# Kernel optimization log

Measured on AMD Instinct MI355X. Metric: run time of the kernel, lower is better.

## Reference

```python
import jax, jax.numpy as jnp
import numpy as np

KSIZE = (15, 15)
SIGMA = (3.0, 3.0)


def _gaussian_kernel1d(kernel_size, sigma):
    ksize_half = (kernel_size - 1) * 0.5
    x = jnp.linspace(-ksize_half, ksize_half, kernel_size, dtype=jnp.float32)
    pdf = jnp.exp(-0.5 * (x / sigma) ** 2)
    return pdf / pdf.sum()


def setup_inputs() -> dict:
    key = jax.random.key(0)
    img = jax.random.normal(key, (8192, 8192), dtype=jnp.float32)
    # kernel = outer(kernel1d_y, kernel1d_x), matching torch.mm(y[:,None], x[None,:])
    k1d_x = _gaussian_kernel1d(KSIZE[0], SIGMA[0])
    k1d_y = _gaussian_kernel1d(KSIZE[1], SIGMA[1])
    kernel = jnp.outer(k1d_y, k1d_x)  # [kh, kw]
    return {"input": img, "kernel": kernel, "stride": 1}


def reference(input, kernel, stride):
    # forward(): squeeze -> custom mirror pad (== reflect, excludes edge) -> valid strided conv
    kh, kw = kernel.shape
    ph, pw = kh // 2, kw // 2
    x = jnp.pad(input, ((ph, ph), (pw, pw)), mode="reflect")  # matches the flip-based pad()
    # single-channel 2D cross-correlation, VALID padding, given stride
    out = jax.lax.conv_general_dilated(
        x[None, None, :, :],            # [1,1,H+2ph,W+2pw]
        kernel[None, None, :, :],       # [1,1,kh,kw]
        window_strides=(stride, stride),
        padding="VALID",
    )
    return out[0, 0]
```

## Files before the change

kernel.cpp:

```cpp
#include <hip/hip_runtime.h>

#define IMG_W 8192
#define IMG_H 8192
#define KS 15
#define RAD 7
#define TW 64
#define TH 64
#define BLOCK 256
#define SIN_W (TW + 2*RAD)
#define SIN_H (TH + 2*RAD)
#define SIN_STRIDE 80
#define MID_STRIDE TW

__device__ __forceinline__ int reflect_idx(int p, int n) {
    if (p < 0) p = -p;
    if (p >= n) p = 2 * n - 2 - p;
    return p;
}

__global__ __launch_bounds__(BLOCK)
void gauss15_fused(const float* __restrict__ in,
                   const float* __restrict__ k2d,
                   float* __restrict__ out) {
    __shared__ float s_in[SIN_H * SIN_STRIDE];
    __shared__ float s_mid[SIN_H * MID_STRIDE];
    __shared__ float s_kx[KS];
    __shared__ float s_ky[KS];

    const int t = threadIdx.x;
    const int col0 = blockIdx.x * TW;
    const int row0 = blockIdx.y * TH;

    if (t < KS) {
        float sx = 0.f, sy = 0.f;
        #pragma unroll
        for (int i = 0; i < KS; i++) {
            sx += k2d[i * KS + t];
            sy += k2d[t * KS + i];
        }
        s_kx[t] = sx;
        s_ky[t] = sy;
    }

    for (int idx = t; idx < SIN_H * SIN_W; idx += BLOCK) {
        int r = idx / SIN_W;
        int c = idx - r * SIN_W;
        int gr = reflect_idx(row0 - RAD + r, IMG_H);
        int gc = reflect_idx(col0 - RAD + c, IMG_W);
        s_in[r * SIN_STRIDE + c] = in[gr * IMG_W + gc];
    }
    __syncthreads();

    float kx[KS], ky[KS];
    #pragma unroll
    for (int i = 0; i < KS; i++) { kx[i] = s_kx[i]; ky[i] = s_ky[i]; }

    for (int idx = t; idx < SIN_H * (TW / 4); idx += BLOCK) {
        int r = idx >> 4;
        int cg = idx & 15;
        const float* rowp = &s_in[r * SIN_STRIDE + cg * 4];
        float f[20];
        *(float4*)(f + 0)  = *(const float4*)(rowp + 0);
        *(float4*)(f + 4)  = *(const float4*)(rowp + 4);
        *(float4*)(f + 8)  = *(const float4*)(rowp + 8);
        *(float4*)(f + 12) = *(const float4*)(rowp + 12);
        *(float4*)(f + 16) = *(const float4*)(rowp + 16);
        float a0 = 0.f, a1 = 0.f, a2 = 0.f, a3 = 0.f;
        #pragma unroll
        for (int j = 0; j < KS; j++) {
            float w = kx[j];
            a0 += f[j + 0] * w;
            a1 += f[j + 1] * w;
            a2 += f[j + 2] * w;
            a3 += f[j + 3] * w;
        }
        *(float4*)&s_mid[r * MID_STRIDE + cg * 4] = make_float4(a0, a1, a2, a3);
    }
    __syncthreads();

    const int cg = t & 15;
    const int rg = t >> 4;
    const int c = cg * 4;
    const int r0 = rg * 4;

    float4 acc[4];
    #pragma unroll
    for (int q = 0; q < 4; q++) acc[q] = make_float4(0.f, 0.f, 0.f, 0.f);

    #pragma unroll
    for (int i = 0; i < KS + 3; i++) {
        float4 v = *(const float4*)&s_mid[(r0 + i) * MID_STRIDE + c];
        #pragma unroll
        for (int q = 0; q < 4; q++) {
            int j = i - q;
            if (j >= 0 && j < KS) {
                float w = ky[j];
                acc[q].x += v.x * w;
                acc[q].y += v.y * w;
                acc[q].z += v.z * w;
                acc[q].w += v.w * w;
            }
        }
    }

    #pragma unroll
    for (int q = 0; q < 4; q++) {
        *(float4*)&out[(size_t)(row0 + r0 + q) * IMG_W + col0 + c] = acc[q];
    }
}

extern "C" void kernel_launch(void* const* d_in, const int* in_sizes, int n_in,
                              void* d_out, int out_size, void* d_ws, size_t ws_size,
                              hipStream_t stream) {
    const float* img = (const float*)d_in[0];
    const float* k2d = (const float*)d_in[1];
    float* out = (float*)d_out;

    dim3 grid(IMG_W / TW, IMG_H / TH);
    gauss15_fused<<<grid, BLOCK, 0, stream>>>(img, k2d, out);
}
```

Baseline: 518.7 us.

## Replace shared-memory tiled separable conv with register-streaming row kernel

Each thread now owns 4 output columns across a 1024-wide by 64-tall block. It streams input rows straight from global memory and does the horizontal pass in registers. The vertical pass uses a 15-entry rotating float4 accumulator ring kept in registers. This drops the shared-memory staging, both __syncthreads, and the intermediate buffer, and reduces the halo overhead, which was about 1.5x reads on 64x64 tiles. The costs are heavy register pressure and a grid of only 1024 blocks, and it relies on L1/L2 to serve the overlapping column reads between neighbouring threads.

```diff
diff --git a/kernel.cpp b/kernel.cpp
--- a/kernel.cpp
+++ b/kernel.cpp
@@ -4,13 +4,9 @@
 #define IMG_H 8192
 #define KS 15
 #define RAD 7
-#define TW 64
-#define TH 64
+#define TW_BLK 1024
+#define TH_BLK 64
 #define BLOCK 256
-#define SIN_W (TW + 2*RAD)
-#define SIN_H (TH + 2*RAD)
-#define SIN_STRIDE 80
-#define MID_STRIDE TW
 
 __device__ __forceinline__ int reflect_idx(int p, int n) {
     if (p < 0) p = -p;
@@ -18,95 +14,128 @@
     return p;
 }
 
-__global__ __launch_bounds__(BLOCK)
-void gauss15_fused(const float* __restrict__ in,
-                   const float* __restrict__ k2d,
-                   float* __restrict__ out) {
-    __shared__ float s_in[SIN_H * SIN_STRIDE];
-    __shared__ float s_mid[SIN_H * MID_STRIDE];
-    __shared__ float s_kx[KS];
-    __shared__ float s_ky[KS];
-
-    const int t = threadIdx.x;
-    const int col0 = blockIdx.x * TW;
-    const int row0 = blockIdx.y * TH;
-
-    if (t < KS) {
-        float sx = 0.f, sy = 0.f;
+template<int K, int JMIN, int JMAX, bool STORE>
+__device__ __forceinline__ void row_body(const float* __restrict__ in,
+                                         float* __restrict__ out,
+                                         int gr, int gcol0, bool safe,
+                                         const float* __restrict__ kxs,
+                                         const float* __restrict__ kys,
+                                         float4* __restrict__ acc,
+                                         int out_off) {
+    const float* __restrict__ rowp = in + ((unsigned)gr << 13);
+    float f[20];
+    if (safe) {
         #pragma unroll
-        for (int i = 0; i < KS; i++) {
-            sx += k2d[i * KS + t];
-            sy += k2d[t * KS + i];
-        }
-        s_kx[t] = sx;
-        s_ky[t] = sy;
+        for (int e = 0; e < 5; ++e)
+            *(float4*)(f + 4 * e) = *(const float4*)(rowp + gcol0 + 4 * e);
+    } else {
+        #pragma unroll
+        for (int e = 0; e < 20; ++e)
+            f[e] = rowp[reflect_idx(gcol0 + e, IMG_W)];
     }
 
-    for (int idx = t; idx < SIN_H * SIN_W; idx += BLOCK) {
-        int r = idx / SIN_W;
-        int c = idx - r * SIN_W;
-        int gr = reflect_idx(row0 - RAD + r, IMG_H);
-        int gc = reflect_idx(col0 - RAD + c, IMG_W);
-        s_in[r * SIN_STRIDE + c] = in[gr * IMG_W + gc];
-    }
-    __syncthreads();
-
-    float kx[KS], ky[KS];
+    float m0 = 0.f, m1 = 0.f, m2 = 0.f, m3 = 0.f;
     #pragma unroll
-    for (int i = 0; i < KS; i++) { kx[i] = s_kx[i]; ky[i] = s_ky[i]; }
-
-    for (int idx = t; idx < SIN_H * (TW / 4); idx += BLOCK) {
-        int r = idx >> 4;
-        int cg = idx & 15;
-        const float* rowp = &s_in[r * SIN_STRIDE + cg * 4];
-        float f[20];
-        *(float4*)(f + 0)  = *(const float4*)(rowp + 0);
-        *(float4*)(f + 4)  = *(const float4*)(rowp + 4);
-        *(float4*)(f + 8)  = *(const float4*)(rowp + 8);
-        *(float4*)(f + 12) = *(const float4*)(rowp + 12);
-        *(float4*)(f + 16) = *(const float4*)(rowp + 16);
-        float a0 = 0.f, a1 = 0.f, a2 = 0.f, a3 = 0.f;
-        #pragma unroll
-        for (int j = 0; j < KS; j++) {
-            float w = kx[j];
-            a0 += f[j + 0] * w;
-            a1 += f[j + 1] * w;
-            a2 += f[j + 2] * w;
-            a3 += f[j + 3] * w;
-        }
-        *(float4*)&s_mid[r * MID_STRIDE + cg * 4] = make_float4(a0, a1, a2, a3);
-    }
-    __syncthreads();
-
-    const int cg = t & 15;
-    const int rg = t >> 4;
-    const int c = cg * 4;
-    const int r0 = rg * 4;
-
-    float4 acc[4];
-    #pragma unroll
-    for (int q = 0; q < 4; q++) acc[q] = make_float4(0.f, 0.f, 0.f, 0.f);
-
-    #pragma unroll
-    for (int i = 0; i < KS + 3; i++) {
-        float4 v = *(const float4*)&s_mid[(r0 + i) * MID_STRIDE + c];
-        #pragma unroll
-        for (int q = 0; q < 4; q++) {
-            int j = i - q;
-            if (j >= 0 && j < KS) {
-                float w = ky[j];
-                acc[q].x += v.x * w;
-                acc[q].y += v.y * w;
-                acc[q].z += v.z * w;
-                acc[q].w += v.w * w;
-            }
-        }
+    for (int j = 0; j < KS; ++j) {
+        const float w = kxs[j];
+        m0 = fmaf(f[1 + j], w, m0);
+        m1 = fmaf(f[2 + j], w, m1);
+        m2 = fmaf(f[3 + j], w, m2);
+        m3 = fmaf(f[4 + j], w, m3);
     }
 
     #pragma unroll
-    for (int q = 0; q < 4; q++) {
-        *(float4*)&out[(size_t)(row0 + r0 + q) * IMG_W + col0 + c] = acc[q];
+    for (int j = JMIN; j <= JMAX; ++j) {
+        const int s = (K - j + KS) % KS;
+        const float w = kys[j];
+        acc[s].x = fmaf(m0, w, acc[s].x);
+        acc[s].y = fmaf(m1, w, acc[s].y);
+        acc[s].z = fmaf(m2, w, acc[s].z);
+        acc[s].w = fmaf(m3, w, acc[s].w);
     }
+
+    if (STORE) {
+        const int s = (K + 1) % KS;
+        *(float4*)(out + out_off) = acc[s];
+        acc[s] = make_float4(0.f, 0.f, 0.f, 0.f);
+    }
+}
+
+__global__ __launch_bounds__(BLOCK, 4)
+void gauss15_stream(const float* __restrict__ in,
+                    const float* __restrict__ k2d,
+                    float* __restrict__ out) {
+    const int t  = threadIdx.x;
+    const int c0 = blockIdx.x * TW_BLK;
+    const int r0 = blockIdx.y * TH_BLK;
+
+    float kxs[KS], kys[KS];
+    #pragma unroll
+    for (int j = 0; j < KS; ++j) {
+        float sx = 0.f, sy = 0.f;
+        #pragma unroll
+        for (int i = 0; i < KS; ++i) {
+            sx += k2d[i * KS + j];
+            sy += k2d[j * KS + i];
+        }
+        kxs[j] = __uint_as_float(__builtin_amdgcn_readfirstlane(__float_as_uint(sx)));
+        kys[j] = __uint_as_float(__builtin_amdgcn_readfirstlane(__float_as_uint(sy)));
+    }
+
+    const int gcol0 = c0 + 4 * t - 8;
+    const bool safe = (gcol0 >= 0) && (gcol0 + 19 < IMG_W);
+
+    float4 acc[KS];
+    #pragma unroll
+    for (int s = 0; s < KS; ++s) acc[s] = make_float4(0.f, 0.f, 0.f, 0.f);
+
+    int out_off = r0 * IMG_W + c0 + 4 * t;
+
+    #define GR(mm) reflect_idx(r0 - RAD + (mm), IMG_H)
+
+    row_body< 0,0, 0,false>(in,out,GR( 0),gcol0,safe,kxs,kys,acc,0);
+    row_body< 1,0, 1,false>(in,out,GR( 1),gcol0,safe,kxs,kys,acc,0);
+    row_body< 2,0, 2,false>(in,out,GR( 2),gcol0,safe,kxs,kys,acc,0);
+    row_body< 3,0, 3,false>(in,out,GR( 3),gcol0,safe,kxs,kys,acc,0);
+    row_body< 4,0, 4,false>(in,out,GR( 4),gcol0,safe,kxs,kys,acc,0);
+    row_body< 5,0, 5,false>(in,out,GR( 5),gcol0,safe,kxs,kys,acc,0);
+    row_body< 6,0, 6,false>(in,out,GR( 6),gcol0,safe,kxs,kys,acc,0);
+    row_body< 7,0, 7,false>(in,out,GR( 7),gcol0,safe,kxs,kys,acc,0);
+    row_body< 8,0, 8,false>(in,out,GR( 8),gcol0,safe,kxs,kys,acc,0);
+    row_body< 9,0, 9,false>(in,out,GR( 9),gcol0,safe,kxs,kys,acc,0);
+    row_body<10,0,10,false>(in,out,GR(10),gcol0,safe,kxs,kys,acc,0);
+    row_body<11,0,11,false>(in,out,GR(11),gcol0,safe,kxs,kys,acc,0);
+    row_body<12,0,12,false>(in,out,GR(12),gcol0,safe,kxs,kys,acc,0);
+    row_body<13,0,13,false>(in,out,GR(13),gcol0,safe,kxs,kys,acc,0);
+
+    row_body<14,0,14,true >(in,out,GR(14),gcol0,safe,kxs,kys,acc,out_off);
+    out_off += IMG_W;
+
+    #pragma unroll 1
+    for (int ch = 0; ch < 4; ++ch) {
+        const int mb = 15 + ch * 15;
+        row_body< 0,0,14,true>(in,out,GR(mb+ 0),gcol0,safe,kxs,kys,acc,out_off); out_off += IMG_W;
+        row_body< 1,0,14,true>(in,out,GR(mb+ 1),gcol0,safe,kxs,kys,acc,out_off); out_off += IMG_W;
+        row_body< 2,0,14,true>(in,out,GR(mb+ 2),gcol0,safe,kxs,kys,acc,out_off); out_off += IMG_W;
+        row_body< 3,0,14,true>(in,out,GR(mb+ 3),gcol0,safe,kxs,kys,acc,out_off); out_off += IMG_W;
+        row_body< 4,0,14,true>(in,out,GR(mb+ 4),gcol0,safe,kxs,kys,acc,out_off); out_off += IMG_W;
+        row_body< 5,0,14,true>(in,out,GR(mb+ 5),gcol0,safe,kxs,kys,acc,out_off); out_off += IMG_W;
+        row_body< 6,0,14,true>(in,out,GR(mb+ 6),gcol0,safe,kxs,kys,acc,out_off); out_off += IMG_W;
+        row_body< 7,0,14,true>(in,out,GR(mb+ 7),gcol0,safe,kxs,kys,acc,out_off); out_off += IMG_W;
+        row_body< 8,0,14,true>(in,out,GR(mb+ 8),gcol0,safe,kxs,kys,acc,out_off); out_off += IMG_W;
+        row_body< 9,0,14,true>(in,out,GR(mb+ 9),gcol0,safe,kxs,kys,acc,out_off); out_off += IMG_W;
+        row_body<10,0,14,true>(in,out,GR(mb+10),gcol0,safe,kxs,kys,acc,out_off); out_off += IMG_W;
+        row_body<11,0,14,true>(in,out,GR(mb+11),gcol0,safe,kxs,kys,acc,out_off); out_off += IMG_W;
+        row_body<12,0,14,true>(in,out,GR(mb+12),gcol0,safe,kxs,kys,acc,out_off); out_off += IMG_W;
+        row_body<13,0,14,true>(in,out,GR(mb+13),gcol0,safe,kxs,kys,acc,out_off); out_off += IMG_W;
+        row_body<14,0,14,true>(in,out,GR(mb+14),gcol0,safe,kxs,kys,acc,out_off); out_off += IMG_W;
+    }
+
+    row_body< 0,12,14,true>(in,out,GR(75),gcol0,safe,kxs,kys,acc,out_off); out_off += IMG_W;
+    row_body< 1,13,14,true>(in,out,GR(76),gcol0,safe,kxs,kys,acc,out_off); out_off += IMG_W;
+    row_body< 2,14,14,true>(in,out,GR(77),gcol0,safe,kxs,kys,acc,out_off);
+
+    #undef GR
 }
 
 extern "C" void kernel_launch(void* const* d_in, const int* in_sizes, int n_in,
@@ -116,6 +145,6 @@
     const float* k2d = (const float*)d_in[1];
     float* out = (float*)d_out;
 
-    dim3 grid(IMG_W / TW, IMG_H / TH);
-    gauss15_fused<<<grid, BLOCK, 0, stream>>>(img, k2d, out);
+    dim3 grid(IMG_W / TW_BLK, IMG_H / TH_BLK);
+    gauss15_stream<<<grid, BLOCK, 0, stream>>>(img, k2d, out);
 }
```

After: 1.014 ms. 95.4% more time.
